# Kernel tuning notes

Measured on AMD Instinct MI355X. Metric: run time of the kernel, lower is better.

Reference implementation:

```python
import jax, jax.numpy as jnp
import numpy as np

NHEAD = 8
NPTS = 4

def _bilinear_sample(E_flat, locs, H, W):
    # E_flat: [B, H*W, D] channel-last flattened feature map
    # locs:   [B, N, 2] normalized (x, y) in [-1, 1], align_corners=False, zeros padding
    ix = ((locs[..., 0] + 1.0) * W - 1.0) * 0.5
    iy = ((locs[..., 1] + 1.0) * H - 1.0) * 0.5
    x0 = jnp.floor(ix); y0 = jnp.floor(iy)
    x1 = x0 + 1.0;      y1 = y0 + 1.0
    wx1 = ix - x0; wx0 = 1.0 - wx1
    wy1 = iy - y0; wy0 = 1.0 - wy1
    gather = jax.vmap(lambda e, i: e[i])  # per-batch gather -> [B, N, D]
    def corner(xc, yc, w):
        valid = (xc >= 0) & (xc < W) & (yc >= 0) & (yc < H)
        xi = jnp.clip(xc, 0, W - 1).astype(jnp.int32)
        yi = jnp.clip(yc, 0, H - 1).astype(jnp.int32)
        g = gather(E_flat, yi * W + xi)
        return g * (w * valid)[..., None]
    return (corner(x0, y0, wx0 * wy0) + corner(x1, y0, wx1 * wy0)
            + corner(x0, y1, wx0 * wy1) + corner(x1, y1, wx1 * wy1))

def setup_inputs() -> dict:
    key = jax.random.key(0)
    ks = jax.random.split(key, 6)
    B, M, D = 8, 1024, 256
    H, Wd = 100, 100
    SADQ = jax.random.normal(ks[0], (B, M, D), jnp.float32)
    E = jax.random.normal(ks[1], (B, H * Wd, D), jnp.float32)
    # learned params (random instead of the degenerate zero-init, so the math is exercised)
    Wo = jax.random.normal(ks[2], (D, NHEAD * NPTS * 2), jnp.float32) * 0.02
    bo = jnp.zeros((NHEAD * NPTS * 2,), jnp.float32)
    Wa = jax.random.normal(ks[3], (D, NHEAD * NPTS), jnp.float32) * 0.05
    ba = jnp.zeros((NHEAD * NPTS,), jnp.float32)
    Wr = jax.random.normal(ks[4], (D, 2), jnp.float32) * 0.05
    br = jnp.zeros((2,), jnp.float32)
    Wp = jax.random.normal(ks[5], (D, D), jnp.float32) * 0.05
    bp = jnp.zeros((D,), jnp.float32)
    return {"SADQ": SADQ, "E": E, "Wo": Wo, "bo": bo, "Wa": Wa, "ba": ba,
            "Wr": Wr, "br": br, "Wp": Wp, "bp": bp, "H": H, "W": Wd}

def reference(SADQ, E, Wo, bo, Wa, ba, Wr, br, Wp, bp, H, W):
    B, M, D = SADQ.shape
    offsets = (SADQ @ Wo + bo).reshape(B, M, NHEAD, NPTS, 2)
    attn = jax.nn.softmax((SADQ @ Wa + ba).reshape(B, M, NHEAD, NPTS), axis=-1)
    base_ref = (SADQ @ Wr + br)[:, :, None, None, :]            # [B, M, 1, 1, 2]
    locs = (base_ref + offsets * 0.1).reshape(B, M * NHEAD * NPTS, 2)
    sampled = _bilinear_sample(E, locs, H, W).reshape(B, M, NHEAD, NPTS, D)
    # sum over points, mean over heads, fused into one contraction
    agg = jnp.einsum('bmhpd,bmhp->bmd', sampled, attn) / NHEAD
    return agg @ Wp + bp
```

## Files before the change

### kernel.cpp

```cpp
#include <hip/hip_runtime.h>
#include <hip/hip_bf16.h>
#include <math.h>

#define BATCH 8
#define MQ    1024
#define DIM   256
#define NHEAD 8
#define NPTS  4
#define NPROJ 98
#define NCORN (NHEAD * NPTS * 4)

__global__ __launch_bounds__(256) void fused_sample_kernel(
    const float* __restrict__ SADQ,
    const float* __restrict__ E,
    const float* __restrict__ Wo, const float* __restrict__ bo,
    const float* __restrict__ Wa, const float* __restrict__ ba,
    const float* __restrict__ Wr, const float* __restrict__ br,
    const int*   __restrict__ Hp, const int* __restrict__ Wdp,
    float* __restrict__ agg)
{
    const int row = blockIdx.x;
    const int b   = row / MQ;
    const int tid = threadIdx.x;

    __shared__ float  qs[DIM];
    __shared__ float  proj[128];
    __shared__ float  partial[128];
    __shared__ float  sW[NCORN];
    __shared__ int    sIdx[NCORN];
    __shared__ float4 red[4][64];

    qs[tid] = SADQ[(size_t)row * DIM + tid];
    __syncthreads();

    {
        const int j    = tid & 127;
        const int half = tid >> 7;
        float s = 0.f, bias = 0.f;
        if (j < NPROJ) {
            const float* Wb; int col, ncols;
            if (j < 64)      { Wb = Wo; col = j;      ncols = 64; bias = bo[col]; }
            else if (j < 96) { Wb = Wa; col = j - 64; ncols = 32; bias = ba[col]; }
            else             { Wb = Wr; col = j - 96; ncols = 2;  bias = br[col]; }
            const float* wp = Wb + (size_t)(half * 128) * ncols + col;
            const float* qp = qs + half * 128;
            #pragma unroll 8
            for (int d = 0; d < 128; ++d)
                s = fmaf(qp[d], wp[(size_t)d * ncols], s);
        }
        if (half) partial[j] = s;
        __syncthreads();
        if (!half && j < NPROJ) proj[j] = s + bias + partial[j];
        __syncthreads();
    }

    const int Hh = *Hp;
    const int Ww = *Wdp;
    if (tid < NHEAD * NPTS) {
        const int p = tid;
        const int h = p >> 2;
        const float l0 = proj[64 + h * 4 + 0];
        const float l1 = proj[64 + h * 4 + 1];
        const float l2 = proj[64 + h * 4 + 2];
        const float l3 = proj[64 + h * 4 + 3];
        const float mx = fmaxf(fmaxf(l0, l1), fmaxf(l2, l3));
        const float e0 = expf(l0 - mx), e1 = expf(l1 - mx),
                    e2 = expf(l2 - mx), e3 = expf(l3 - mx);
        const float inv = 1.f / (e0 + e1 + e2 + e3);
        const float aw  = expf(proj[64 + p] - mx) * inv * (1.f / NHEAD);

        const float lx = proj[96] + 0.1f * proj[p * 2 + 0];
        const float ly = proj[97] + 0.1f * proj[p * 2 + 1];
        const float ix = ((lx + 1.f) * (float)Ww - 1.f) * 0.5f;
        const float iy = ((ly + 1.f) * (float)Hh - 1.f) * 0.5f;
        const float x0f = floorf(ix), y0f = floorf(iy);
        const int   x0  = (int)x0f,   y0  = (int)y0f;
        const float wx1 = ix - x0f, wx0 = 1.f - wx1;
        const float wy1 = iy - y0f, wy0 = 1.f - wy1;

        #pragma unroll
        for (int c = 0; c < 4; ++c) {
            const int   xc = x0 + (c & 1);
            const int   yc = y0 + (c >> 1);
            const float wx = (c & 1) ? wx1 : wx0;
            const float wy = (c >> 1) ? wy1 : wy0;
            const bool valid = (xc >= 0) && (xc < Ww) && (yc >= 0) && (yc < Hh);
            const int xi = min(max(xc, 0), Ww - 1);
            const int yi = min(max(yc, 0), Hh - 1);
            sW  [p * 4 + c] = valid ? (wx * wy * aw) : 0.f;
            sIdx[p * 4 + c] = (yi * Ww + xi) * (DIM / 4);
        }
    }
    __syncthreads();

    const int cg  = tid >> 6;
    const int ch4 = tid & 63;
    const float4* __restrict__ Eb4 =
        (const float4*)(E + (size_t)b * (size_t)(Hh * Ww) * DIM);

    float4 acc = make_float4(0.f, 0.f, 0.f, 0.f);
    #pragma unroll
    for (int t = 0; t < 32; ++t) {
        const int   i   = cg * 32 + t;
        const float w   = sW[i];
        const int   idx = sIdx[i];
        const float4 e  = Eb4[(size_t)idx + ch4];
        acc.x = fmaf(w, e.x, acc.x);
        acc.y = fmaf(w, e.y, acc.y);
        acc.z = fmaf(w, e.z, acc.z);
        acc.w = fmaf(w, e.w, acc.w);
    }
    red[cg][ch4] = acc;
    __syncthreads();

    if (cg == 0) {
        const float4 r0 = red[0][ch4];
        const float4 r1 = red[1][ch4];
        const float4 r2 = red[2][ch4];
        const float4 r3 = red[3][ch4];
        float4 o;
        o.x = (r0.x + r1.x) + (r2.x + r3.x);
        o.y = (r0.y + r1.y) + (r2.y + r3.y);
        o.z = (r0.z + r1.z) + (r2.z + r3.z);
        o.w = (r0.w + r1.w) + (r2.w + r3.w);
        *(float4*)&agg[(size_t)row * DIM + ch4 * 4] = o;
    }
}

__global__ __launch_bounds__(256) void proj_gemm_kernel(
    const float* __restrict__ A,
    const float* __restrict__ Wp,
    const float* __restrict__ bp,
    float* __restrict__ out)
{
    __shared__ float As[16][64];
    __shared__ float Bs[16][64];

    const int tid = threadIdx.x;
    const int mb  = blockIdx.x * 64;
    const int nb  = blockIdx.y * 64;
    const int tm  = (tid >> 4) << 2;
    const int tn  = (tid & 15) << 2;

    float acc[4][4] = {};

    for (int kb = 0; kb < DIM; kb += 16) {
        {
            const int m  = tid & 63;
            const int k0 = (tid >> 6) << 2;
            const float4 v = *(const float4*)&A[(size_t)(mb + m) * DIM + kb + k0];
            As[k0 + 0][m] = v.x; As[k0 + 1][m] = v.y;
            As[k0 + 2][m] = v.z; As[k0 + 3][m] = v.w;
            const int k = tid >> 4;
            const int n = (tid & 15) << 2;
            *(float4*)&Bs[k][n] = *(const float4*)&Wp[(size_t)(kb + k) * DIM + nb + n];
        }
        __syncthreads();

        #pragma unroll
        for (int k = 0; k < 16; ++k) {
            const float4 a  = *(const float4*)&As[k][tm];
            const float4 b4 = *(const float4*)&Bs[k][tn];
            acc[0][0] = fmaf(a.x, b4.x, acc[0][0]);
            acc[0][1] = fmaf(a.x, b4.y, acc[0][1]);
            acc[0][2] = fmaf(a.x, b4.z, acc[0][2]);
            acc[0][3] = fmaf(a.x, b4.w, acc[0][3]);
            acc[1][0] = fmaf(a.y, b4.x, acc[1][0]);
            acc[1][1] = fmaf(a.y, b4.y, acc[1][1]);
            acc[1][2] = fmaf(a.y, b4.z, acc[1][2]);
            acc[1][3] = fmaf(a.y, b4.w, acc[1][3]);
            acc[2][0] = fmaf(a.z, b4.x, acc[2][0]);
            acc[2][1] = fmaf(a.z, b4.y, acc[2][1]);
            acc[2][2] = fmaf(a.z, b4.z, acc[2][2]);
            acc[2][3] = fmaf(a.z, b4.w, acc[2][3]);
            acc[3][0] = fmaf(a.w, b4.x, acc[3][0]);
            acc[3][1] = fmaf(a.w, b4.y, acc[3][1]);
            acc[3][2] = fmaf(a.w, b4.z, acc[3][2]);
            acc[3][3] = fmaf(a.w, b4.w, acc[3][3]);
        }
        __syncthreads();
    }

    const float4 bv = *(const float4*)&bp[nb + tn];
    #pragma unroll
    for (int i = 0; i < 4; ++i) {
        float4 o;
        o.x = acc[i][0] + bv.x;
        o.y = acc[i][1] + bv.y;
        o.z = acc[i][2] + bv.z;
        o.w = acc[i][3] + bv.w;
        *(float4*)&out[(size_t)(mb + tm + i) * DIM + nb + tn] = o;
    }
}

extern "C" void kernel_launch(void* const* d_in, const int* in_sizes, int n_in,
                              void* d_out, int out_size, void* d_ws, size_t ws_size,
                              hipStream_t stream)
{
    const float* SADQ = (const float*)d_in[0];
    const float* E    = (const float*)d_in[1];
    const float* Wo   = (const float*)d_in[2];
    const float* bo   = (const float*)d_in[3];
    const float* Wa   = (const float*)d_in[4];
    const float* ba   = (const float*)d_in[5];
    const float* Wr   = (const float*)d_in[6];
    const float* br   = (const float*)d_in[7];
    const float* Wp   = (const float*)d_in[8];
    const float* bp   = (const float*)d_in[9];
    const int*   Hp   = (const int*)d_in[10];
    const int*   Wdp  = (const int*)d_in[11];

    float* agg = (float*)d_ws;
    float* out = (float*)d_out;

    const int BM = in_sizes[0] / DIM;

    fused_sample_kernel<<<BM, 256, 0, stream>>>(
        SADQ, E, Wo, bo, Wa, ba, Wr, br, Hp, Wdp, agg);

    dim3 g2(BM / 64, DIM / 64);
    proj_gemm_kernel<<<g2, 256, 0, stream>>>(agg, Wp, bp, out);
}
```

Baseline: 229.5 us.

## Run output projection as bf16 MFMA GEMM with bf16 intermediate

The sampling kernel now writes its aggregated features as bf16 instead of fp32, which halves the intermediate write and read traffic. A new kernel converts and transposes Wp to bf16 on every call. The fp32 FMA tiled GEMM is replaced by an MFMA 16x16x32 bf16 kernel that stages 64x32 tiles in LDS. This lowers the precision of the final projection and adds an extra small kernel launch.

```diff
diff --git a/kernel.cpp b/kernel.cpp
--- a/kernel.cpp
+++ b/kernel.cpp
@@ -10,6 +10,15 @@
 #define NPROJ 98
 #define NCORN (NHEAD * NPTS * 4)
 
+typedef __attribute__((ext_vector_type(8))) short  short8;
+typedef __attribute__((ext_vector_type(4))) float  f32x4;
+
+static __device__ __forceinline__ ushort f2bf(float f) {
+    union { float f; unsigned u; } v; v.f = f;
+    const unsigned r = v.u + 0x7fffu + ((v.u >> 16) & 1u);
+    return (ushort)(r >> 16);
+}
+
 __global__ __launch_bounds__(256) void fused_sample_kernel(
     const float* __restrict__ SADQ,
     const float* __restrict__ E,
@@ -17,7 +26,7 @@
     const float* __restrict__ Wa, const float* __restrict__ ba,
     const float* __restrict__ Wr, const float* __restrict__ br,
     const int*   __restrict__ Hp, const int* __restrict__ Wdp,
-    float* __restrict__ agg)
+    ushort* __restrict__ aggb)
 {
     const int row = blockIdx.x;
     const int b   = row / MQ;
@@ -118,78 +127,79 @@
         const float4 r1 = red[1][ch4];
         const float4 r2 = red[2][ch4];
         const float4 r3 = red[3][ch4];
-        float4 o;
-        o.x = (r0.x + r1.x) + (r2.x + r3.x);
-        o.y = (r0.y + r1.y) + (r2.y + r3.y);
-        o.z = (r0.z + r1.z) + (r2.z + r3.z);
-        o.w = (r0.w + r1.w) + (r2.w + r3.w);
-        *(float4*)&agg[(size_t)row * DIM + ch4 * 4] = o;
-    }
-}
-
-__global__ __launch_bounds__(256) void proj_gemm_kernel(
-    const float* __restrict__ A,
-    const float* __restrict__ Wp,
-    const float* __restrict__ bp,
+        ushort4 o;
+        o.x = f2bf((r0.x + r1.x) + (r2.x + r3.x));
+        o.y = f2bf((r0.y + r1.y) + (r2.y + r3.y));
+        o.z = f2bf((r0.z + r1.z) + (r2.z + r3.z));
+        o.w = f2bf((r0.w + r1.w) + (r2.w + r3.w));
+        *(ushort4*)&aggb[(size_t)row * DIM + ch4 * 4] = o;
+    }
+}
+
+__global__ __launch_bounds__(256) void wp_convert_kernel(
+    const float* __restrict__ Wp, ushort* __restrict__ WpT)
+{
+    const int k = blockIdx.x;
+    const int n = threadIdx.x;
+    WpT[(size_t)n * DIM + k] = f2bf(Wp[(size_t)k * DIM + n]);
+}
+
+__global__ __launch_bounds__(256) void mfma_gemm_kernel(
+    const ushort* __restrict__ A,
+    const ushort* __restrict__ BT,
+    const float*  __restrict__ bp,
     float* __restrict__ out)
 {
-    __shared__ float As[16][64];
-    __shared__ float Bs[16][64];
-
-    const int tid = threadIdx.x;
-    const int mb  = blockIdx.x * 64;
-    const int nb  = blockIdx.y * 64;
-    const int tm  = (tid >> 4) << 2;
-    const int tn  = (tid & 15) << 2;
-
-    float acc[4][4] = {};
-
-    for (int kb = 0; kb < DIM; kb += 16) {
-        {
-            const int m  = tid & 63;
-            const int k0 = (tid >> 6) << 2;
-            const float4 v = *(const float4*)&A[(size_t)(mb + m) * DIM + kb + k0];
-            As[k0 + 0][m] = v.x; As[k0 + 1][m] = v.y;
-            As[k0 + 2][m] = v.z; As[k0 + 3][m] = v.w;
-            const int k = tid >> 4;
-            const int n = (tid & 15) << 2;
-            *(float4*)&Bs[k][n] = *(const float4*)&Wp[(size_t)(kb + k) * DIM + nb + n];
-        }
-        __syncthreads();
-
-        #pragma unroll
-        for (int k = 0; k < 16; ++k) {
-            const float4 a  = *(const float4*)&As[k][tm];
-            const float4 b4 = *(const float4*)&Bs[k][tn];
-            acc[0][0] = fmaf(a.x, b4.x, acc[0][0]);
-            acc[0][1] = fmaf(a.x, b4.y, acc[0][1]);
-            acc[0][2] = fmaf(a.x, b4.z, acc[0][2]);
-            acc[0][3] = fmaf(a.x, b4.w, acc[0][3]);
-            acc[1][0] = fmaf(a.y, b4.x, acc[1][0]);
-            acc[1][1] = fmaf(a.y, b4.y, acc[1][1]);
-            acc[1][2] = fmaf(a.y, b4.z, acc[1][2]);
-            acc[1][3] = fmaf(a.y, b4.w, acc[1][3]);
-            acc[2][0] = fmaf(a.z, b4.x, acc[2][0]);
-            acc[2][1] = fmaf(a.z, b4.y, acc[2][1]);
-            acc[2][2] = fmaf(a.z, b4.z, acc[2][2]);
-            acc[2][3] = fmaf(a.z, b4.w, acc[2][3]);
-            acc[3][0] = fmaf(a.w, b4.x, acc[3][0]);
-            acc[3][1] = fmaf(a.w, b4.y, acc[3][1]);
-            acc[3][2] = fmaf(a.w, b4.z, acc[3][2]);
-            acc[3][3] = fmaf(a.w, b4.w, acc[3][3]);
-        }
-        __syncthreads();
-    }
-
-    const float4 bv = *(const float4*)&bp[nb + tn];
+    __shared__ ushort ldsA[64 * 40];
+    __shared__ ushort ldsB[64 * 40];
+
+    const int tid  = threadIdx.x;
+    const int mb   = blockIdx.x * 64;
+    const int nb   = blockIdx.y * 64;
+    const int wave = tid >> 6;
+    const int lane = tid & 63;
+    const int r0   = (wave >> 1) * 32;
+    const int c0   = (wave & 1) * 32;
+    const int lrow = lane & 15;
+    const int kgrp = lane >> 4;
+
+    const int sm = tid >> 2;
+    const int sc = (tid & 3) * 8;
+
+    f32x4 acc00 = {0.f, 0.f, 0.f, 0.f};
+    f32x4 acc01 = {0.f, 0.f, 0.f, 0.f};
+    f32x4 acc10 = {0.f, 0.f, 0.f, 0.f};
+    f32x4 acc11 = {0.f, 0.f, 0.f, 0.f};
+
+    for (int kb = 0; kb < DIM; kb += 32) {
+        *(uint4*)&ldsA[sm * 40 + sc] =
+            *(const uint4*)&A[(size_t)(mb + sm) * DIM + kb + sc];
+        *(uint4*)&ldsB[sm * 40 + sc] =
+            *(const uint4*)&BT[(size_t)(nb + sm) * DIM + kb + sc];
+        __syncthreads();
+
+        const short8 a0 = *(const short8*)&ldsA[(r0 + lrow)      * 40 + kgrp * 8];
+        const short8 a1 = *(const short8*)&ldsA[(r0 + 16 + lrow) * 40 + kgrp * 8];
+        const short8 b0 = *(const short8*)&ldsB[(c0 + lrow)      * 40 + kgrp * 8];
+        const short8 b1 = *(const short8*)&ldsB[(c0 + 16 + lrow) * 40 + kgrp * 8];
+
+        acc00 = __builtin_amdgcn_mfma_f32_16x16x32_bf16(a0, b0, acc00, 0, 0, 0);
+        acc01 = __builtin_amdgcn_mfma_f32_16x16x32_bf16(a0, b1, acc01, 0, 0, 0);
+        acc10 = __builtin_amdgcn_mfma_f32_16x16x32_bf16(a1, b0, acc10, 0, 0, 0);
+        acc11 = __builtin_amdgcn_mfma_f32_16x16x32_bf16(a1, b1, acc11, 0, 0, 0);
+        __syncthreads();
+    }
+
+    const int orow = mb + r0 + kgrp * 4;
+    const int ocol = nb + c0 + lrow;
+    const float bp0 = bp[ocol];
+    const float bp1 = bp[ocol + 16];
     #pragma unroll
-    for (int i = 0; i < 4; ++i) {
-        float4 o;
-        o.x = acc[i][0] + bv.x;
-        o.y = acc[i][1] + bv.y;
-        o.z = acc[i][2] + bv.z;
-        o.w = acc[i][3] + bv.w;
-        *(float4*)&out[(size_t)(mb + tm + i) * DIM + nb + tn] = o;
+    for (int reg = 0; reg < 4; ++reg) {
+        out[(size_t)(orow + reg)      * DIM + ocol]      = acc00[reg] + bp0;
+        out[(size_t)(orow + reg)      * DIM + ocol + 16] = acc01[reg] + bp1;
+        out[(size_t)(orow + 16 + reg) * DIM + ocol]      = acc10[reg] + bp0;
+        out[(size_t)(orow + 16 + reg) * DIM + ocol + 16] = acc11[reg] + bp1;
     }
 }
 
@@ -210,14 +220,17 @@
     const int*   Hp   = (const int*)d_in[10];
     const int*   Wdp  = (const int*)d_in[11];
 
-    float* agg = (float*)d_ws;
-    float* out = (float*)d_out;
-
     const int BM = in_sizes[0] / DIM;
 
+    ushort* aggb = (ushort*)d_ws;
+    ushort* WpT  = (ushort*)((char*)d_ws + (size_t)BM * DIM * 2);
+    float*  out  = (float*)d_out;
+
     fused_sample_kernel<<<BM, 256, 0, stream>>>(
-        SADQ, E, Wo, bo, Wa, ba, Wr, br, Hp, Wdp, agg);
+        SADQ, E, Wo, bo, Wa, ba, Wr, br, Hp, Wdp, aggb);
+
+    wp_convert_kernel<<<DIM, 256, 0, stream>>>(Wp, WpT);
 
     dim3 g2(BM / 64, DIM / 64);
-    proj_gemm_kernel<<<g2, 256, 0, stream>>>(agg, Wp, bp, out);
-}
+    mfma_gemm_kernel<<<g2, 256, 0, stream>>>(aggb, WpT, bp, out);
+}
```

Measured after the change: 216.2 us. 1.06x faster.
